# Optimization experiments

Measured on AMD Instinct MI355X. Metric: run time of the kernel, lower is better.

The kernel has to match this reference:

```python
import jax, jax.numpy as jnp
import numpy as np
import math

N, C, T, V = 32, 64, 400, 27
S = 2            # num_subset
IC = 16          # inter_channels
EPS = 1e-5


def _spatial_pe(channels, num_node):
    # PositionalEncoding(domain='spatial'): pe[c, t, v] depends only on joint id v
    pos = jnp.arange(num_node, dtype=jnp.float32)                      # [V]
    div = jnp.exp(jnp.arange(0, channels, 2, dtype=jnp.float32)
                  * (-math.log(10000.0) / channels))                   # [C/2]
    ang = div[:, None] * pos[None, :]                                  # [C/2, V]
    pe = jnp.stack([jnp.sin(ang), jnp.cos(ang)], axis=1)               # [C/2, 2, V]
    return pe.reshape(channels, num_node)                              # [C, V]


def _conv1x1(x, w, b):
    # x: [N, Cin, T, V], w: [Cout, Cin]
    return jnp.einsum('nctv,oc->notv', x, w) + b[None, :, None, None]


def _bn(x, g, b, m, v):
    inv = g / jnp.sqrt(v + EPS)
    return x * inv[None, :, None, None] + (b - m * inv)[None, :, None, None]


def _leaky(x):
    return jnp.where(x >= 0, x, 0.1 * x)


def setup_inputs() -> dict:
    key = jax.random.key(0)
    ks = jax.random.split(key, 24)
    d = {}
    d['x'] = jax.random.normal(ks[0], (N, C, T, V), jnp.float32)
    d['w_in'] = jax.random.normal(ks[1], (2 * S * IC, C), jnp.float32) * 0.1
    d['b_in'] = jax.random.normal(ks[2], (2 * S * IC,), jnp.float32) * 0.05
    d['alphas'] = jnp.ones((1, S, 1, 1), jnp.float32)
    d['att0'] = jax.random.uniform(ks[3], (1, S, V, V), jnp.float32) / V
    d['w_outs'] = jax.random.normal(ks[4], (C, S * C), jnp.float32) * 0.08
    d['b_outs'] = jax.random.normal(ks[5], (C,), jnp.float32) * 0.05
    d['bn_outs_g'] = jax.random.uniform(ks[6], (C,), jnp.float32) + 0.5
    d['bn_outs_b'] = jax.random.normal(ks[7], (C,), jnp.float32) * 0.05
    d['bn_outs_m'] = jax.random.normal(ks[8], (C,), jnp.float32) * 0.1
    d['bn_outs_v'] = jax.random.uniform(ks[9], (C,), jnp.float32) + 0.5
    d['w_ff'] = jax.random.normal(ks[10], (C, C), jnp.float32) * 0.1
    d['b_ff'] = jax.random.normal(ks[11], (C,), jnp.float32) * 0.05
    d['bn_ff_g'] = jax.random.uniform(ks[12], (C,), jnp.float32) + 0.5
    d['bn_ff_b'] = jax.random.normal(ks[13], (C,), jnp.float32) * 0.05
    d['bn_ff_m'] = jax.random.normal(ks[14], (C,), jnp.float32) * 0.1
    d['bn_ff_v'] = jax.random.uniform(ks[15], (C,), jnp.float32) + 0.5
    d['w_t'] = jax.random.normal(ks[16], (C, C, 3, 1), jnp.float32) * 0.08
    d['b_t'] = jax.random.normal(ks[17], (C,), jnp.float32) * 0.05
    d['bn_t_g'] = jax.random.uniform(ks[18], (C,), jnp.float32) + 0.5
    d['bn_t_b'] = jax.random.normal(ks[19], (C,), jnp.float32) * 0.05
    d['bn_t_m'] = jax.random.normal(ks[20], (C,), jnp.float32) * 0.1
    d['bn_t_v'] = jax.random.uniform(ks[21], (C,), jnp.float32) + 0.5
    return d


def reference(x, w_in, b_in, alphas, att0,
              w_outs, b_outs, bn_outs_g, bn_outs_b, bn_outs_m, bn_outs_v,
              w_ff, b_ff, bn_ff_g, bn_ff_b, bn_ff_m, bn_ff_v,
              w_t, b_t, bn_t_g, bn_t_b, bn_t_m, bn_t_v):
    n, c, t, v = x.shape
    # spatial positional encoding (broadcast over T)
    pe = _spatial_pe(c, v)                                      # [C, V]
    y = x + pe[None, :, None, :]
    # q/k projection: 1x1 conv -> [N, 2S, IC, T, V], chunk on subset axis
    qk = _conv1x1(y, w_in, b_in).reshape(n, 2 * S, IC, t, v)
    q, k = qk[:, :S], qk[:, S:]
    # tanh attention over joints + learnable global bias (atts buffer is zeros)
    att = jnp.tanh(jnp.einsum('nsctu,nsctv->nsuv', q, k) / (IC * t)) * alphas
    att = att + att0                                            # [N, S, V, V]
    # aggregate V-dim: [N, S, C, T, V] -> [N, S*C, T, V]
    y = jnp.einsum('nctu,nsuv->nsctv', x, att).reshape(n, S * c, t, v)
    y = _bn(_conv1x1(y, w_outs, b_outs), bn_outs_g, bn_outs_b, bn_outs_m, bn_outs_v)
    y = _leaky(x + y)                                           # downs1 = identity
    y2 = _bn(_conv1x1(y, w_ff, b_ff), bn_ff_g, bn_ff_b, bn_ff_m, bn_ff_v)
    y2 = _leaky(x + y2)                                         # downs2 = identity
    # temporal conv (3,1), padding (1,0), stride 1
    z = jax.lax.conv_general_dilated(
        y2, w_t, window_strides=(1, 1), padding=((1, 1), (0, 0)),
        dimension_numbers=('NCHW', 'OIHW', 'NCHW')) + b_t[None, :, None, None]
    z = _bn(z, bn_t_g, bn_t_b, bn_t_m, bn_t_v)
    z = _leaky(y2 + z)                                          # downt2 = identity
    return z
```

## Files before the change

### kernel.cpp

```cpp
#include <hip/hip_runtime.h>
#include <hip/hip_bf16.h>
#include <math.h>


typedef __hip_bfloat16 bf16;
typedef unsigned short u16t;
typedef unsigned int u32t;

using bf16x8 = __attribute__((ext_vector_type(8))) short;
using f32x4  = __attribute__((ext_vector_type(4))) float;

#define NN 32
#define CH 64
#define TT 400
#define VV 27
#define PIX 10800
#define NSUV (32*2*27*27)
#define XTOT (NN*CH*PIX)

#define TB1 4
#define NT1 100
#define TB2 4
#define NT2 100
#define TBS 9
#define NTS 45

__device__ __forceinline__ float lrelu(float x) { return x >= 0.f ? x : 0.1f * x; }
__device__ __forceinline__ float4 ld4(const float* p) { return *reinterpret_cast<const float4*>(p); }
__device__ __forceinline__ uint2 ld2u(const u32t* p) { return *reinterpret_cast<const uint2*>(p); }

__device__ __forceinline__ u16t f2bf(float f) {
    return __bfloat16_as_ushort(__float2bfloat16(f));
}
__device__ __forceinline__ u32t packbf(float lo, float hi) {
    return ((u32t)f2bf(hi) << 16) | (u32t)f2bf(lo);
}
__device__ __forceinline__ float bf2f(u16t u) {
    return __uint_as_float(((u32t)u) << 16);
}
__device__ __forceinline__ u32t cvtpk(float lo, float hi) {
    u32t r;
    asm("v_cvt_pk_bf16_f32 %0, %1, %2" : "=v"(r) : "v"(lo), "v"(hi));
    return r;
}
__device__ __forceinline__ void dot2v(float& c, u32t a, u32t b) {
    asm("v_dot2_f32_bf16 %0, %1, %2, %0" : "+v"(c) : "v"(a), "v"(b));
}
__device__ __forceinline__ void dot2s(float& c, u32t a_sgpr, u32t b) {
    asm("v_dot2_f32_bf16 %0, %1, %2, %0" : "+v"(c) : "s"(a_sgpr), "v"(b));
}

__global__ void k_prep(
    const float* __restrict__ w_outs, const float* __restrict__ b_outs,
    const float* __restrict__ go, const float* __restrict__ bo,
    const float* __restrict__ mo, const float* __restrict__ vo,
    const float* __restrict__ w_ff, const float* __restrict__ b_ff,
    const float* __restrict__ gf, const float* __restrict__ bf,
    const float* __restrict__ mf, const float* __restrict__ vf,
    const float* __restrict__ w_t, const float* __restrict__ b_t,
    const float* __restrict__ gt, const float* __restrict__ btb,
    const float* __restrict__ mt, const float* __restrict__ vt,
    const float* __restrict__ w_in,
    u16t* __restrict__ wfoA, float* __restrict__ bfo,
    u16t* __restrict__ wffA, float* __restrict__ bff,
    u16t* __restrict__ wtA, float* __restrict__ bft,
    u32t* __restrict__ wqkpk)
{
    const int total = 8192 + 4096 + 12288 + 192 + 2048;
    for (int idx = blockIdx.x * 256 + threadIdx.x; idx < total; idx += gridDim.x * 256) {
        if (idx < 8192) {
            int o = idx >> 7, j = idx & 127;
            float inv = go[o] * rsqrtf(vo[o] + 1e-5f);
            wfoA[idx] = f2bf(w_outs[o * 128 + j] * inv);
        } else if (idx < 12288) {
            int r = idx - 8192; int o = r >> 6, c = r & 63;
            float inv = gf[o] * rsqrtf(vf[o] + 1e-5f);
            wffA[r] = f2bf(w_ff[o * 64 + c] * inv);
        } else if (idx < 24576) {
            int r = idx - 12288;
            int o = r / 192, k2 = r % 192;
            int kt = k2 >> 6, c = k2 & 63;
            float inv = gt[o] * rsqrtf(vt[o] + 1e-5f);
            wtA[r] = f2bf(w_t[o * 192 + c * 3 + kt] * inv);
        } else if (idx < 24768) {
            int r = idx - 24576; int o = r & 63, which = r >> 6;
            if (which == 0) {
                float inv = go[o] * rsqrtf(vo[o] + 1e-5f);
                bfo[o] = b_outs[o] * inv + bo[o] - mo[o] * inv;
            } else if (which == 1) {
                float inv = gf[o] * rsqrtf(vf[o] + 1e-5f);
                bff[o] = b_ff[o] * inv + bf[o] - mf[o] * inv;
            } else {
                float inv = gt[o] * rsqrtf(vt[o] + 1e-5f);
                bft[o] = b_t[o] * inv + btb[o] - mt[o] * inv;
            }
        } else {
            int i = idx - 24768;
            int cc2 = i & 31, c = (i >> 5) & 15, sq = i >> 9;
            int s = sq >> 1, qk = sq & 1;
            int row = qk * 32 + s * 16 + c;
            wqkpk[i] = packbf(w_in[row * 64 + 2 * cc2], w_in[row * 64 + 2 * cc2 + 1]);
        }
    }
}

__global__ __launch_bounds__(256) void k_pbias(
    const float* __restrict__ w_in, const float* __restrict__ b_in,
    float* __restrict__ pb)
{
    __shared__ float pe[64 * 27];
    const int tid = threadIdx.x;
    for (int idx = tid; idx < 1728; idx += 256) {
        int c = idx / 27, u = idx % 27;
        float div = expf(-0.28782313662425575f * (float)(c >> 1));
        float ang = div * (float)u;
        pe[idx] = (c & 1) ? cosf(ang) : sinf(ang);
    }
    __syncthreads();
    for (int idx = tid; idx < 1792; idx += 256) {
        int u = idx % 28, r = idx / 28;
        int c = r % 16, sq = r / 16;
        if (u >= 27) { pb[idx] = 0.f; continue; }
        int s = sq >> 1, qk = sq & 1;
        int row = qk * 32 + s * 16 + c;
        float acc = b_in[row];
        for (int cc = 0; cc < 64; ++cc) acc += w_in[row * 64 + cc] * pe[cc * 27 + u];
        pb[idx] = acc;
    }
}

__global__ __launch_bounds__(256, 4) void k_scores(
    const float* __restrict__ x, const u32t* __restrict__ wqkpk,
    const float* __restrict__ pb, float* __restrict__ scores)
{
    const int tid = threadIdx.x;
    const int s = blockIdx.y, n = blockIdx.z;
    const int t0 = blockIdx.x * TBS;

    __shared__ u32t qlds[TBS * 27 * 10];
    __shared__ u32t klds[TBS * 27 * 10];

    const int pcl = tid < 243 ? tid : 242;
    const int tt = pcl / 27, u = pcl - tt * 27;
    const int t = t0 + tt;
    const bool valid = (tid < 243) && (t < TT);

    u32t xp[32];
    const float* xb = x + (size_t)n * 64 * PIX + (size_t)(t < TT ? t : 0) * 27 + u;
    #pragma unroll
    for (int c2 = 0; c2 < 32; ++c2) {
        float v0 = xb[(size_t)(2 * c2) * PIX];
        float v1 = xb[(size_t)(2 * c2 + 1) * PIX];
        xp[c2] = cvtpk(v0, v1);
    }

    const float* pbq = pb + ((s * 2 + 0) * 16) * 28 + u;
    const float* pbk = pb + ((s * 2 + 1) * 16) * 28 + u;
    const u32t* wq = wqkpk + (s * 2 + 0) * 16 * 32;
    const u32t* wk = wqkpk + (s * 2 + 1) * 16 * 32;
    float qr[16], kr[16];
    #pragma unroll
    for (int c = 0; c < 16; ++c) { qr[c] = pbq[c * 28]; kr[c] = pbk[c * 28]; }
    #pragma unroll
    for (int c = 0; c < 16; ++c) {
        const u32t* wr = wq + c * 32;
        #pragma unroll
        for (int c2 = 0; c2 < 32; ++c2) dot2s(qr[c], wr[c2], xp[c2]);
    }
    #pragma unroll
    for (int c = 0; c < 16; ++c) {
        const u32t* wr = wk + c * 32;
        #pragma unroll
        for (int c2 = 0; c2 < 32; ++c2) dot2s(kr[c], wr[c2], xp[c2]);
    }

    if (tid < 243) {
        #pragma unroll
        for (int c2 = 0; c2 < 8; ++c2) {
            qlds[(tt * 27 + u) * 10 + c2] = valid ? cvtpk(qr[2 * c2], qr[2 * c2 + 1]) : 0u;
            klds[(tt * 27 + u) * 10 + c2] = valid ? cvtpk(kr[2 * c2], kr[2 * c2 + 1]) : 0u;
        }
    }
    __syncthreads();

    const int sid = tid < 243 ? tid : 242;
    const int ug = sid / 9, vg = sid % 9;
    const int v0 = vg * 3;
    float sc0 = 0.f, sc1 = 0.f, sc2 = 0.f;
    for (int t2 = 0; t2 < TBS; ++t2) {
        const u32t* qrow = qlds + (t2 * 27 + ug) * 10;
        const u32t* k0 = klds + (t2 * 27 + v0) * 10;
        #pragma unroll
        for (int c4 = 0; c4 < 4; ++c4) {
            uint2 qp = ld2u(qrow + c4 * 2);
            uint2 ka = ld2u(k0 + c4 * 2);
            uint2 kb = ld2u(k0 + 10 + c4 * 2);
            uint2 kc = ld2u(k0 + 20 + c4 * 2);
            dot2v(sc0, qp.x, ka.x); dot2v(sc0, qp.y, ka.y);
            dot2v(sc1, qp.x, kb.x); dot2v(sc1, qp.y, kb.y);
            dot2v(sc2, qp.x, kc.x); dot2v(sc2, qp.y, kc.y);
        }
    }
    if (tid < 243) {
        float* sb = scores + (n * 2 + s) * 729 + ug * 27 + v0;
        atomicAdd(&sb[0], sc0);
        atomicAdd(&sb[1], sc1);
        atomicAdd(&sb[2], sc2);
    }
}

__global__ void k_att(const float* __restrict__ scores,
                      const float* __restrict__ alphas,
                      const float* __restrict__ att0,
                      u32t* __restrict__ attTp)
{
    int i = blockIdx.x * 256 + threadIdx.x;
    if (i >= NN * 2 * 32 * 16) return;
    int e = i & 15;
    int r = i >> 4;
    int v = r & 31;
    int ns = r >> 5;
    int s = ns & 1;
    if (v >= 27) { attTp[i] = 0u; return; }
    const float* sb = scores + ns * 729;
    const float* ab = att0 + s * 729;
    float al = alphas[s];
    int u0 = 2 * e, u1 = 2 * e + 1;
    float a0 = (u0 < 27) ? tanhf(sb[u0 * 27 + v] * (1.f / 6400.f)) * al + ab[u0 * 27 + v] : 0.f;
    float a1 = (u1 < 27) ? tanhf(sb[u1 * 27 + v] * (1.f / 6400.f)) * al + ab[u1 * 27 + v] : 0.f;
    attTp[i] = packbf(a0, a1);
}

__global__ __launch_bounds__(512, 4) void k_stage1(
    const float* __restrict__ x, const u32t* __restrict__ attTp,
    const u16t* __restrict__ wfoA, const float* __restrict__ bfo,
    const u16t* __restrict__ wffA, const float* __restrict__ bff,
    u16t* __restrict__ y2)
{
    const int tid = threadIdx.x;
    const int n = blockIdx.y, t0 = blockIdx.x * TB1;
    const int w = tid >> 6, li = tid & 15, g = (tid >> 4) & 3;

    __shared__ __align__(16) u16t xs[4 * 64 * 32];
    __shared__ __align__(16) u32t mmL[112 * 68];
    __shared__ __align__(16) u32t y1L[112 * 34];

    for (int j = tid; j < 4096; j += 512) {
        int i = j & 15, c = (j >> 4) & 63, tt = j >> 10;
        const float* xrow = x + (size_t)(n * 64 + c) * PIX + (size_t)(t0 + tt) * 27;
        int u0 = 2 * i;
        float v0 = (u0 < 27) ? xrow[u0] : 0.f;
        float v1 = (u0 + 1 < 27) ? xrow[u0 + 1] : 0.f;
        int ip = i ^ (((c >> 1) & 3) << 2);
        reinterpret_cast<u32t*>(xs)[(tt * 64 + c) * 16 + ip] = packbf(v0, v1);
    }
    __syncthreads();

    {
        const int t = w & 3, s = w >> 2;
        bf16x8 ax[4];
        #pragma unroll
        for (int Mt = 0; Mt < 4; ++Mt) {
            const int c = Mt * 16 + li;
            const int blk = g ^ ((li >> 1) & 3);
            ax[Mt] = *reinterpret_cast<const bf16x8*>(&xs[(t * 64 + c) * 32 + blk * 8]);
        }
        const u16t* attp16 = reinterpret_cast<const u16t*>(attTp);
        #pragma unroll
        for (int Nt = 0; Nt < 2; ++Nt) {
            bf16x8 b = *reinterpret_cast<const bf16x8*>(
                &attp16[(((n * 2 + s) * 32) + Nt * 16 + li) * 32 + g * 8]);
            const int v = Nt * 16 + li;
            #pragma unroll
            for (int Mt = 0; Mt < 4; ++Mt) {
                f32x4 d = {0.f, 0.f, 0.f, 0.f};
                d = __builtin_amdgcn_mfma_f32_16x16x32_bf16(ax[Mt], b, d, 0, 0, 0);
                if (v < 28) {
                    const int p = t * 28 + v;
                    const int j2 = s * 32 + Mt * 8 + g * 2;
                    mmL[p * 68 + j2]     = packbf(d[0], d[1]);
                    mmL[p * 68 + j2 + 1] = packbf(d[2], d[3]);
                }
            }
        }
    }
    __syncthreads();

    const int ot = w & 3, hh = w >> 2;
    const int o0 = ot * 16 + g * 4;

    {
        bf16x8 aw[4];
        #pragma unroll
        for (int Ks = 0; Ks < 4; ++Ks)
            aw[Ks] = *reinterpret_cast<const bf16x8*>(&wfoA[(ot * 16 + li) * 128 + Ks * 32 + g * 8]);
        float4 bf4 = ld4(&bfo[o0]);
        #pragma unroll
        for (int q = 0; q < 4; ++q) {
            const int Nt = hh * 4 + q;
            if (Nt >= 7) continue;
            f32x4 d = {0.f, 0.f, 0.f, 0.f};
            #pragma unroll
            for (int Ks = 0; Ks < 4; ++Ks) {
                bf16x8 b = *reinterpret_cast<const bf16x8*>(&mmL[(Nt * 16 + li) * 68 + Ks * 16 + g * 4]);
                d = __builtin_amdgcn_mfma_f32_16x16x32_bf16(aw[Ks], b, d, 0, 0, 0);
            }
            const int p = Nt * 16 + li;
            const int tt = p / 28, v = p - tt * 28;
            const int sw0 = ((o0 >> 1) & 3) << 3;
            const int sw1 = (((o0 + 2) >> 1) & 3) << 3;
            float ya = lrelu(bf2f(xs[(tt * 64 + o0 + 0) * 32 + (v ^ sw0)]) + d[0] + bf4.x);
            float yb = lrelu(bf2f(xs[(tt * 64 + o0 + 1) * 32 + (v ^ sw0)]) + d[1] + bf4.y);
            float yc = lrelu(bf2f(xs[(tt * 64 + o0 + 2) * 32 + (v ^ sw1)]) + d[2] + bf4.z);
            float yd = lrelu(bf2f(xs[(tt * 64 + o0 + 3) * 32 + (v ^ sw1)]) + d[3] + bf4.w);
            y1L[p * 34 + ot * 8 + g * 2]     = packbf(ya, yb);
            y1L[p * 34 + ot * 8 + g * 2 + 1] = packbf(yc, yd);
        }
    }
    __syncthreads();

    {
        bf16x8 af[2];
        #pragma unroll
        for (int Ks = 0; Ks < 2; ++Ks)
            af[Ks] = *reinterpret_cast<const bf16x8*>(&wffA[(ot * 16 + li) * 64 + Ks * 32 + g * 8]);
        float4 bff4 = ld4(&bff[o0]);
        #pragma unroll
        for (int q = 0; q < 4; ++q) {
            const int Nt = hh * 4 + q;
            if (Nt >= 7) continue;
            f32x4 d = {0.f, 0.f, 0.f, 0.f};
            #pragma unroll
            for (int Ks = 0; Ks < 2; ++Ks) {
                union { uint2 u2[2]; bf16x8 v8; } bu;
                bu.u2[0] = *reinterpret_cast<const uint2*>(&y1L[(Nt * 16 + li) * 34 + Ks * 16 + g * 4]);
                bu.u2[1] = *reinterpret_cast<const uint2*>(&y1L[(Nt * 16 + li) * 34 + Ks * 16 + g * 4 + 2]);
                d = __builtin_amdgcn_mfma_f32_16x16x32_bf16(af[Ks], bu.v8, d, 0, 0, 0);
            }
            const int p = Nt * 16 + li;
            const int tt = p / 28, v = p - tt * 28;
            if (v < 27) {
                const int sw0 = ((o0 >> 1) & 3) << 3;
                const int sw1 = (((o0 + 2) >> 1) & 3) << 3;
                u16t* yb0 = y2 + (size_t)(n * 64) * PIX + (size_t)(t0 + tt) * 27 + v;
                yb0[(size_t)(o0 + 0) * PIX] = f2bf(lrelu(bf2f(xs[(tt * 64 + o0 + 0) * 32 + (v ^ sw0)]) + d[0] + bff4.x));
                yb0[(size_t)(o0 + 1) * PIX] = f2bf(lrelu(bf2f(xs[(tt * 64 + o0 + 1) * 32 + (v ^ sw0)]) + d[1] + bff4.y));
                yb0[(size_t)(o0 + 2) * PIX] = f2bf(lrelu(bf2f(xs[(tt * 64 + o0 + 2) * 32 + (v ^ sw1)]) + d[2] + bff4.z));
                yb0[(size_t)(o0 + 3) * PIX] = f2bf(lrelu(bf2f(xs[(tt * 64 + o0 + 3) * 32 + (v ^ sw1)]) + d[3] + bff4.w));
            }
        }
    }
}

__global__ __launch_bounds__(256, 4) void k_stage2(
    const u16t* __restrict__ y2in, const u16t* __restrict__ wtA,
    const float* __restrict__ bft, float* __restrict__ out)
{
    const int tid = threadIdx.x;
    const int n = blockIdx.y, t0 = blockIdx.x * TB2;
    const int w = tid >> 6, li = tid & 15, g = (tid >> 4) & 3;

    __shared__ __align__(16) u16t ys[6 * 28 * 72];

    for (int idx = tid; idx < 6 * 28 * 64; idx += 256) {
        int v = idx % 28, r = idx / 28;
        int tp = r % 6, c = r / 6;
        int t = t0 - 1 + tp;
        ys[(tp * 28 + v) * 72 + c] = (v < 27 && t >= 0 && t < TT)
            ? y2in[(size_t)(n * 64 + c) * PIX + t * 27 + v] : (u16t)0;
    }
    __syncthreads();

    const int o0 = w * 16 + g * 4;
    bf16x8 aw[6];
    #pragma unroll
    for (int Ks = 0; Ks < 6; ++Ks)
        aw[Ks] = *reinterpret_cast<const bf16x8*>(&wtA[(w * 16 + li) * 192 + Ks * 32 + g * 8]);
    float4 bt4 = ld4(&bft[o0]);

    #pragma unroll
    for (int Nt = 0; Nt < 7; ++Nt) {
        const int p = Nt * 16 + li;
        const int tt = p / 28, v = p - tt * 28;
        f32x4 d = {0.f, 0.f, 0.f, 0.f};
        #pragma unroll
        for (int Ks = 0; Ks < 6; ++Ks) {
            const int kt = Ks >> 1, c0 = (Ks & 1) * 32 + g * 8;
            bf16x8 b = *reinterpret_cast<const bf16x8*>(&ys[((tt + kt) * 28 + v) * 72 + c0]);
            d = __builtin_amdgcn_mfma_f32_16x16x32_bf16(aw[Ks], b, d, 0, 0, 0);
        }
        if (v < 27) {
            float* ob = out + (size_t)(n * 64) * PIX + (size_t)(t0 + tt) * 27 + v;
            float r0 = bf2f(ys[((tt + 1) * 28 + v) * 72 + o0 + 0]);
            float r1 = bf2f(ys[((tt + 1) * 28 + v) * 72 + o0 + 1]);
            float r2 = bf2f(ys[((tt + 1) * 28 + v) * 72 + o0 + 2]);
            float r3 = bf2f(ys[((tt + 1) * 28 + v) * 72 + o0 + 3]);
            ob[(size_t)(o0 + 0) * PIX] = lrelu(r0 + d[0] + bt4.x);
            ob[(size_t)(o0 + 1) * PIX] = lrelu(r1 + d[1] + bt4.y);
            ob[(size_t)(o0 + 2) * PIX] = lrelu(r2 + d[2] + bt4.z);
            ob[(size_t)(o0 + 3) * PIX] = lrelu(r3 + d[3] + bt4.w);
        }
    }
}

extern "C" void kernel_launch(void* const* d_in, const int* in_sizes, int n_in,
                              void* d_out, int out_size, void* d_ws, size_t ws_size,
                              hipStream_t stream)
{
    const float* x      = (const float*)d_in[0];
    const float* w_in   = (const float*)d_in[1];
    const float* b_in   = (const float*)d_in[2];
    const float* alphas = (const float*)d_in[3];
    const float* att0   = (const float*)d_in[4];
    const float* w_outs = (const float*)d_in[5];
    const float* b_outs = (const float*)d_in[6];
    const float* bog    = (const float*)d_in[7];
    const float* bob    = (const float*)d_in[8];
    const float* bom    = (const float*)d_in[9];
    const float* bov    = (const float*)d_in[10];
    const float* w_ff   = (const float*)d_in[11];
    const float* b_ff   = (const float*)d_in[12];
    const float* bfg    = (const float*)d_in[13];
    const float* bfb    = (const float*)d_in[14];
    const float* bfm    = (const float*)d_in[15];
    const float* bfv    = (const float*)d_in[16];
    const float* w_t    = (const float*)d_in[17];
    const float* b_t    = (const float*)d_in[18];
    const float* btg    = (const float*)d_in[19];
    const float* btb    = (const float*)d_in[20];
    const float* btm    = (const float*)d_in[21];
    const float* btv    = (const float*)d_in[22];

    float* pbw    = (float*)d_ws;
    float* scores = pbw + 1792;
    u32t*  attTp  = (u32t*)(scores + NSUV);
    u16t*  wfoA   = (u16t*)(attTp + 32768);
    u16t*  wffA   = (u16t*)((u32t*)wfoA + 4096);
    u16t*  wtA    = (u16t*)((u32t*)wffA + 2048);
    float* bfo    = (float*)((u32t*)wtA + 6144);
    float* bff    = bfo + 64;
    float* bft    = bff + 64;
    u32t*  wqkpk  = (u32t*)(bft + 64);
    u16t*  y2     = (u16t*)(wqkpk + 2048);

    hipMemsetAsync(scores, 0, NSUV * sizeof(float), stream);

    k_prep<<<32, 256, 0, stream>>>(w_outs, b_outs, bog, bob, bom, bov,
                                   w_ff, b_ff, bfg, bfb, bfm, bfv,
                                   w_t, b_t, btg, btb, btm, btv, w_in,
                                   wfoA, bfo, wffA, bff, wtA, bft, wqkpk);
    k_pbias<<<1, 256, 0, stream>>>(w_in, b_in, pbw);
    k_scores<<<dim3(NTS, 2, NN), 256, 0, stream>>>(x, wqkpk, pbw, scores);
    k_att<<<(NN * 2 * 32 * 16 + 255) / 256, 256, 0, stream>>>(scores, alphas, att0, attTp);
    k_stage1<<<dim3(NT1, NN), 512, 0, stream>>>(x, attTp, wfoA, bfo, wffA, bff, y2);
    k_stage2<<<dim3(NT2, NN), 256, 0, stream>>>(y2, wtA, bft, (float*)d_out);
}
```

Before: 383.0 us.

## Store intermediate y2 channel-last and read it directly from global in stage2

Stage1 now writes the bf16 intermediate in pixel-major, channel-contiguous layout using packed 8-byte stores instead of four strided 2-byte stores. Stage2 drops its shared-memory staging tile and the barrier, loading 16-byte channel vectors straight from global memory as MFMA B operands, with clamped indices and zero-masking for temporal padding. Occupancy hint for stage2 is raised. This removes the LDS transpose and the scattered stores, at the cost of redundant global/L2 reads across the three temporal taps and the overlapping halo rows.

```diff
diff --git a/kernel.cpp b/kernel.cpp
--- a/kernel.cpp
+++ b/kernel.cpp
@@ -235,7 +235,7 @@
     const float* __restrict__ x, const u32t* __restrict__ attTp,
     const u16t* __restrict__ wfoA, const float* __restrict__ bfo,
     const u16t* __restrict__ wffA, const float* __restrict__ bff,
-    u16t* __restrict__ y2)
+    u16t* __restrict__ y2T)
 {
     const int tid = threadIdx.x;
     const int n = blockIdx.y, t0 = blockIdx.x * TB1;
@@ -342,63 +342,62 @@
             if (v < 27) {
                 const int sw0 = ((o0 >> 1) & 3) << 3;
                 const int sw1 = (((o0 + 2) >> 1) & 3) << 3;
-                u16t* yb0 = y2 + (size_t)(n * 64) * PIX + (size_t)(t0 + tt) * 27 + v;
-                yb0[(size_t)(o0 + 0) * PIX] = f2bf(lrelu(bf2f(xs[(tt * 64 + o0 + 0) * 32 + (v ^ sw0)]) + d[0] + bff4.x));
-                yb0[(size_t)(o0 + 1) * PIX] = f2bf(lrelu(bf2f(xs[(tt * 64 + o0 + 1) * 32 + (v ^ sw0)]) + d[1] + bff4.y));
-                yb0[(size_t)(o0 + 2) * PIX] = f2bf(lrelu(bf2f(xs[(tt * 64 + o0 + 2) * 32 + (v ^ sw1)]) + d[2] + bff4.z));
-                yb0[(size_t)(o0 + 3) * PIX] = f2bf(lrelu(bf2f(xs[(tt * 64 + o0 + 3) * 32 + (v ^ sw1)]) + d[3] + bff4.w));
+                float r0 = lrelu(bf2f(xs[(tt * 64 + o0 + 0) * 32 + (v ^ sw0)]) + d[0] + bff4.x);
+                float r1 = lrelu(bf2f(xs[(tt * 64 + o0 + 1) * 32 + (v ^ sw0)]) + d[1] + bff4.y);
+                float r2 = lrelu(bf2f(xs[(tt * 64 + o0 + 2) * 32 + (v ^ sw1)]) + d[2] + bff4.z);
+                float r3 = lrelu(bf2f(xs[(tt * 64 + o0 + 3) * 32 + (v ^ sw1)]) + d[3] + bff4.w);
+                uint2 st;
+                st.x = packbf(r0, r1);
+                st.y = packbf(r2, r3);
+                size_t P = (size_t)n * PIX + (size_t)(t0 + tt) * 27 + v;
+                *reinterpret_cast<uint2*>(y2T + P * 64 + o0) = st;
             }
         }
     }
 }
 
-__global__ __launch_bounds__(256, 4) void k_stage2(
-    const u16t* __restrict__ y2in, const u16t* __restrict__ wtA,
+__global__ __launch_bounds__(256, 8) void k_stage2(
+    const u16t* __restrict__ y2T, const u16t* __restrict__ wtA,
     const float* __restrict__ bft, float* __restrict__ out)
 {
     const int tid = threadIdx.x;
     const int n = blockIdx.y, t0 = blockIdx.x * TB2;
     const int w = tid >> 6, li = tid & 15, g = (tid >> 4) & 3;
-
-    __shared__ __align__(16) u16t ys[6 * 28 * 72];
-
-    for (int idx = tid; idx < 6 * 28 * 64; idx += 256) {
-        int v = idx % 28, r = idx / 28;
-        int tp = r % 6, c = r / 6;
-        int t = t0 - 1 + tp;
-        ys[(tp * 28 + v) * 72 + c] = (v < 27 && t >= 0 && t < TT)
-            ? y2in[(size_t)(n * 64 + c) * PIX + t * 27 + v] : (u16t)0;
-    }
-    __syncthreads();
-
     const int o0 = w * 16 + g * 4;
+
+    const u16t* yb = y2T + (size_t)n * PIX * 64;
+
     bf16x8 aw[6];
     #pragma unroll
     for (int Ks = 0; Ks < 6; ++Ks)
         aw[Ks] = *reinterpret_cast<const bf16x8*>(&wtA[(w * 16 + li) * 192 + Ks * 32 + g * 8]);
     float4 bt4 = ld4(&bft[o0]);
+    const bf16x8 bz = {0, 0, 0, 0, 0, 0, 0, 0};
 
     #pragma unroll
     for (int Nt = 0; Nt < 7; ++Nt) {
         const int p = Nt * 16 + li;
         const int tt = p / 28, v = p - tt * 28;
+        const int vc = v < 27 ? v : 26;
         f32x4 d = {0.f, 0.f, 0.f, 0.f};
         #pragma unroll
         for (int Ks = 0; Ks < 6; ++Ks) {
             const int kt = Ks >> 1, c0 = (Ks & 1) * 32 + g * 8;
-            bf16x8 b = *reinterpret_cast<const bf16x8*>(&ys[((tt + kt) * 28 + v) * 72 + c0]);
+            const int tk = t0 + tt + kt - 1;
+            const bool ok = (v < 27) && (tk >= 0) && (tk < TT);
+            const int tkc = tk < 0 ? 0 : (tk >= TT ? TT - 1 : tk);
+            bf16x8 b = *reinterpret_cast<const bf16x8*>(&yb[((size_t)tkc * 27 + vc) * 64 + c0]);
+            b = ok ? b : bz;
             d = __builtin_amdgcn_mfma_f32_16x16x32_bf16(aw[Ks], b, d, 0, 0, 0);
         }
         if (v < 27) {
-            float* ob = out + (size_t)(n * 64) * PIX + (size_t)(t0 + tt) * 27 + v;
-            float r0 = bf2f(ys[((tt + 1) * 28 + v) * 72 + o0 + 0]);
-            float r1 = bf2f(ys[((tt + 1) * 28 + v) * 72 + o0 + 1]);
-            float r2 = bf2f(ys[((tt + 1) * 28 + v) * 72 + o0 + 2]);
-            float r3 = bf2f(ys[((tt + 1) * 28 + v) * 72 + o0 + 3]);
-            ob[(size_t)(o0 + 0) * PIX] = lrelu(r0 + d[0] + bt4.x);
-            ob[(size_t)(o0 + 1) * PIX] = lrelu(r1 + d[1] + bt4.y);
-            ob[(size_t)(o0 + 2) * PIX] = lrelu(r2 + d[2] + bt4.z);
-            ob[(size_t)(o0 + 3) * PIX] = lrelu(r3 + d[3] + bt4.w);
+            const size_t Pq = (size_t)(t0 + tt) * 27 + v;
+            uint2 rv = *reinterpret_cast<const uint2*>(&yb[Pq * 64 + o0]);
+            float* ob = out + (size_t)(n * 64) * PIX + Pq;
+            ob[(size_t)(o0 + 0) * PIX] = lrelu(bf2f((u16t)(rv.x & 0xffff)) + d[0] + bt4.x);
+            ob[(size_t)(o0 + 1) * PIX] = lrelu(bf2f((u16t)(rv.x >> 16))    + d[1] + bt4.y);
+            ob[(size_t)(o0 + 2) * PIX] = lrelu(bf2f((u16t)(rv.y & 0xffff)) + d[2] + bt4.z);
+            ob[(size_t)(o0 + 3) * PIX] = lrelu(bf2f((u16t)(rv.y >> 16))    + d[3] + bt4.w);
         }
     }
 }
@@ -441,7 +440,7 @@
     float* bff    = bfo + 64;
     float* bft    = bff + 64;
     u32t*  wqkpk  = (u32t*)(bft + 64);
-    u16t*  y2     = (u16t*)(wqkpk + 2048);
+    u16t*  y2T    = (u16t*)(wqkpk + 2048);
 
     hipMemsetAsync(scores, 0, NSUV * sizeof(float), stream);
 
@@ -452,6 +451,6 @@
     k_pbias<<<1, 256, 0, stream>>>(w_in, b_in, pbw);
     k_scores<<<dim3(NTS, 2, NN), 256, 0, stream>>>(x, wqkpk, pbw, scores);
     k_att<<<(NN * 2 * 32 * 16 + 255) / 256, 256, 0, stream>>>(scores, alphas, att0, attTp);
-    k_stage1<<<dim3(NT1, NN), 512, 0, stream>>>(x, attTp, wfoA, bfo, wffA, bff, y2);
-    k_stage2<<<dim3(NT2, NN), 256, 0, stream>>>(y2, wtA, bft, (float*)d_out);
-}
+    k_stage1<<<dim3(NT1, NN), 512, 0, stream>>>(x, attTp, wfoA, bfo, wffA, bff, y2T);
+    k_stage2<<<dim3(NT2, NN), 256, 0, stream>>>(y2T, wtA, bft, (float*)d_out);
+}
```

Result: slower. 433.8 us (+13.3%).

## Store intermediate y2 channel-last so both kernels use vectorized accesses

Applied to the files above, without the earlier changes.

The intermediate activation between the two stage kernels moves from NCHW (channel-strided) to a pixel-major, channel-contiguous layout. Stage1 now writes four channels per lane as a single 8-byte store instead of four scattered 2-byte stores. Stage2 loads 16-byte vectors of 8 channels straight into its LDS tile and zero-fills the padding column separately. This is meant to cut uncoalesced global traffic on the intermediate; stage1 stores are still strided across pixels within a wavefront.

```diff
diff --git a/kernel.cpp b/kernel.cpp
--- a/kernel.cpp
+++ b/kernel.cpp
@@ -235,7 +235,7 @@
     const float* __restrict__ x, const u32t* __restrict__ attTp,
     const u16t* __restrict__ wfoA, const float* __restrict__ bfo,
     const u16t* __restrict__ wffA, const float* __restrict__ bff,
-    u16t* __restrict__ y2)
+    u16t* __restrict__ y2T)
 {
     const int tid = threadIdx.x;
     const int n = blockIdx.y, t0 = blockIdx.x * TB1;
@@ -342,18 +342,22 @@
             if (v < 27) {
                 const int sw0 = ((o0 >> 1) & 3) << 3;
                 const int sw1 = (((o0 + 2) >> 1) & 3) << 3;
-                u16t* yb0 = y2 + (size_t)(n * 64) * PIX + (size_t)(t0 + tt) * 27 + v;
-                yb0[(size_t)(o0 + 0) * PIX] = f2bf(lrelu(bf2f(xs[(tt * 64 + o0 + 0) * 32 + (v ^ sw0)]) + d[0] + bff4.x));
-                yb0[(size_t)(o0 + 1) * PIX] = f2bf(lrelu(bf2f(xs[(tt * 64 + o0 + 1) * 32 + (v ^ sw0)]) + d[1] + bff4.y));
-                yb0[(size_t)(o0 + 2) * PIX] = f2bf(lrelu(bf2f(xs[(tt * 64 + o0 + 2) * 32 + (v ^ sw1)]) + d[2] + bff4.z));
-                yb0[(size_t)(o0 + 3) * PIX] = f2bf(lrelu(bf2f(xs[(tt * 64 + o0 + 3) * 32 + (v ^ sw1)]) + d[3] + bff4.w));
+                float r0 = lrelu(bf2f(xs[(tt * 64 + o0 + 0) * 32 + (v ^ sw0)]) + d[0] + bff4.x);
+                float r1 = lrelu(bf2f(xs[(tt * 64 + o0 + 1) * 32 + (v ^ sw0)]) + d[1] + bff4.y);
+                float r2 = lrelu(bf2f(xs[(tt * 64 + o0 + 2) * 32 + (v ^ sw1)]) + d[2] + bff4.z);
+                float r3 = lrelu(bf2f(xs[(tt * 64 + o0 + 3) * 32 + (v ^ sw1)]) + d[3] + bff4.w);
+                uint2 st;
+                st.x = packbf(r0, r1);
+                st.y = packbf(r2, r3);
+                size_t P = (size_t)n * PIX + (size_t)(t0 + tt) * 27 + v;
+                *reinterpret_cast<uint2*>(y2T + P * 64 + o0) = st;
             }
         }
     }
 }
 
 __global__ __launch_bounds__(256, 4) void k_stage2(
-    const u16t* __restrict__ y2in, const u16t* __restrict__ wtA,
+    const u16t* __restrict__ y2T, const u16t* __restrict__ wtA,
     const float* __restrict__ bft, float* __restrict__ out)
 {
     const int tid = threadIdx.x;
@@ -362,12 +366,20 @@
 
     __shared__ __align__(16) u16t ys[6 * 28 * 72];
 
-    for (int idx = tid; idx < 6 * 28 * 64; idx += 256) {
-        int v = idx % 28, r = idx / 28;
-        int tp = r % 6, c = r / 6;
+    for (int idx = tid; idx < 6 * 27 * 8; idx += 256) {
+        int q = idx & 7, r = idx >> 3;
+        int v = r % 27, tp = r / 27;
         int t = t0 - 1 + tp;
-        ys[(tp * 28 + v) * 72 + c] = (v < 27 && t >= 0 && t < TT)
-            ? y2in[(size_t)(n * 64 + c) * PIX + t * 27 + v] : (u16t)0;
+        uint4 val = {0u, 0u, 0u, 0u};
+        if (t >= 0 && t < TT)
+            val = *reinterpret_cast<const uint4*>(
+                &y2T[((size_t)n * PIX + (size_t)t * 27 + v) * 64 + q * 8]);
+        *reinterpret_cast<uint4*>(&ys[(tp * 28 + v) * 72 + q * 8]) = val;
+    }
+    for (int idx = tid; idx < 6 * 8; idx += 256) {
+        int q = idx & 7, tp = idx >> 3;
+        uint4 z = {0u, 0u, 0u, 0u};
+        *reinterpret_cast<uint4*>(&ys[(tp * 28 + 27) * 72 + q * 8]) = z;
     }
     __syncthreads();
 
@@ -441,7 +453,7 @@
     float* bff    = bfo + 64;
     float* bft    = bff + 64;
     u32t*  wqkpk  = (u32t*)(bft + 64);
-    u16t*  y2     = (u16t*)(wqkpk + 2048);
+    u16t*  y2T    = (u16t*)(wqkpk + 2048);
 
     hipMemsetAsync(scores, 0, NSUV * sizeof(float), stream);
 
@@ -452,6 +464,6 @@
     k_pbias<<<1, 256, 0, stream>>>(w_in, b_in, pbw);
     k_scores<<<dim3(NTS, 2, NN), 256, 0, stream>>>(x, wqkpk, pbw, scores);
     k_att<<<(NN * 2 * 32 * 16 + 255) / 256, 256, 0, stream>>>(scores, alphas, att0, attTp);
-    k_stage1<<<dim3(NT1, NN), 512, 0, stream>>>(x, attTp, wfoA, bfo, wffA, bff, y2);
-    k_stage2<<<dim3(NT2, NN), 256, 0, stream>>>(y2, wtA, bft, (float*)d_out);
-}
+    k_stage1<<<dim3(NT1, NN), 512, 0, stream>>>(x, attTp, wfoA, bfo, wffA, bff, y2T);
+    k_stage2<<<dim3(NT2, NN), 256, 0, stream>>>(y2T, wtA, bft, (float*)d_out);
+}
```

Result: faster. 355.2 us (-7.3%).
